# Performance work log

Hardware: AMD Instinct MI355X
Metric: run time of the kernel (lower is better)

## Reference

```python
import jax, jax.numpy as jnp
import numpy as np
from jax import lax

S = 3000      # number of stocks (and number of targets)
F = 6         # raw features
N = 128       # hidden size
L = 40        # lookback length
L_MAX = 10    # max lag
K = 5         # topk leaders


def setup_inputs() -> dict:
    key = jax.random.key(0)
    ks = jax.random.split(key, 16)
    sc = 1.0 / np.sqrt(N)
    u = lambda k, shp, s=sc: jax.random.uniform(k, shp, jnp.float32, -s, s)
    return {
        "X_scaled": jax.random.normal(ks[0], (1, S, L, F), jnp.float32),
        "X_raw": jax.random.normal(ks[1], (1, S, L, F), jnp.float32),
        "target_idx": jax.random.randint(ks[2], (S,), 0, S, jnp.int32),
        "lstm_Wih": u(ks[3], (4 * N, F)),
        "lstm_Whh": u(ks[4], (4 * N, N)),
        "lstm_bih": u(ks[5], (4 * N,)),
        "lstm_bhh": u(ks[6], (4 * N,)),
        "ln_g": jnp.ones((N,), jnp.float32),
        "ln_b": jnp.zeros((N,), jnp.float32),
        "WQ": u(ks[7], (N, N)),
        "WK": u(ks[8], (N, N)),
        "log_temp": jnp.asarray(np.log(N ** 0.25), jnp.float32),
        "lag_bias": jnp.zeros((L_MAX,), jnp.float32),
        "W1": u(ks[9], (64, 2 * F), 1.0 / np.sqrt(2 * F)),
        "b1": jnp.zeros((64,), jnp.float32),
        "W2": u(ks[10], (32, 64), 1.0 / 8.0),
        "b2": jnp.zeros((32,), jnp.float32),
        "W3": u(ks[11], (1, 32), 1.0 / np.sqrt(32)),
        "b3": jnp.zeros((1,), jnp.float32),
    }


def _lstm(x, Wih, Whh, bih, bhh):
    # x: [BS, L, F] -> hidden sequence [BS, L, N]; torch gate order i,f,g,o
    BS = x.shape[0]
    h0 = jnp.zeros((BS, N), x.dtype)
    bias = bih + bhh

    def step(carry, xt):
        h, c = carry
        g = xt @ Wih.T + h @ Whh.T + bias
        i, f, gg, o = jnp.split(g, 4, axis=-1)
        c = jax.nn.sigmoid(f) * c + jax.nn.sigmoid(i) * jnp.tanh(gg)
        h = jax.nn.sigmoid(o) * jnp.tanh(c)
        return (h, c), h

    _, hs = lax.scan(step, (h0, h0), jnp.swapaxes(x, 0, 1))
    return jnp.swapaxes(hs, 0, 1)


def _ln(x, g, b):
    m = x.mean(-1, keepdims=True)
    v = ((x - m) ** 2).mean(-1, keepdims=True)
    return (x - m) / jnp.sqrt(v + 1e-5) * g + b


def _l2norm(x):
    return x / jnp.clip(jnp.linalg.norm(x, axis=-1, keepdims=True), 1e-12)


def reference(X_scaled, X_raw, target_idx, lstm_Wih, lstm_Whh, lstm_bih,
              lstm_bhh, ln_g, ln_b, WQ, WK, log_temp, lag_bias,
              W1, b1, W2, b2, W3, b3):
    # TemporalEncoder: LSTM over B*S sequences + LayerNorm (B=1)
    H = _ln(_lstm(X_scaled.reshape(S, L, F), lstm_Wih, lstm_Whh,
                  lstm_bih, lstm_bhh), ln_g, ln_b)          # [S, L, N]
    X = X_raw[0]                                            # [S, L, F]

    q = _l2norm(H[target_idx, -1] @ WQ.T)                   # [T, N]
    Hk = _l2norm(H[:, L - L_MAX:] @ WK.T)                   # [S, l_max, N]
    temp = jnp.clip(jnp.exp(log_temp), 0.1, N ** 0.5)

    attn = jnp.einsum('tn,sln->tsl', q, Hk) / temp + lag_bias  # [T, S, l_max]
    self_mask = jnp.arange(S)[None, :] == target_idx[:, None]  # [T, S]
    attn = jnp.where(self_mask[:, :, None], -jnp.inf, attn)

    vals, idx = lax.top_k(attn.reshape(-1, S * L_MAX), K)   # [T, K]
    leader = idx // L_MAX
    lag_j = idx % L_MAX
    lag_pos = jnp.clip(L - 1 - (L_MAX - lag_j), 0, L - 1)

    z = X[leader, lag_pos]                                  # [T, K, F]
    w = jax.nn.softmax(vals, axis=1)
    z_agg = (w[..., None] * z).sum(1)                       # [T, F]
    feat = jnp.concatenate([z_agg, z[:, 0]], axis=-1)       # [T, 2F]

    h1 = jax.nn.relu(feat @ W1.T + b1)
    h2 = jax.nn.relu(h1 @ W2.T + b2)
    return (h2 @ W3.T + b3).squeeze(-1)                     # [T]
```

## Files before the change

kernel.cpp:

```cpp
#include <hip/hip_runtime.h>
#include <math.h>

#define S_N 3000
#define NCOLS 30000
#define SCHUNK 16
#define KTILES 938
#define TPC 59
#define PST 17

typedef __bf16 v8bf __attribute__((ext_vector_type(8)));
typedef float v16f __attribute__((ext_vector_type(16)));
typedef float v4f __attribute__((ext_vector_type(4)));

__device__ __forceinline__ float sigm(float x) { return 1.0f / (1.0f + expf(-x)); }

__device__ __forceinline__ bool bet(float av, int ai, float bv, int bi) {
  return (av > bv) || (av == bv && ai < bi);
}

template <int M>
__device__ __forceinline__ void insS(float (&v)[M], int (&ix)[M], float nv, int ni) {
  if (!(nv > v[M - 1])) return;
  bool b[M];
#pragma unroll
  for (int q = 0; q < M; q++) b[q] = nv > v[q];
#pragma unroll
  for (int q = M - 1; q > 0; q--) {
    v[q]  = b[q] ? (b[q - 1] ? v[q - 1] : nv) : v[q];
    ix[q] = b[q] ? (b[q - 1] ? ix[q - 1] : ni) : ix[q];
  }
  if (b[0]) { v[0] = nv; ix[0] = ni; }
}

template <int M>
__device__ __forceinline__ void insF(float (&v)[M], int (&ix)[M], float nv, int ni) {
  if (!bet(nv, ni, v[M - 1], ix[M - 1])) return;
  bool b[M];
#pragma unroll
  for (int q = 0; q < M; q++) b[q] = bet(nv, ni, v[q], ix[q]);
#pragma unroll
  for (int q = M - 1; q > 0; q--) {
    v[q]  = b[q] ? (b[q - 1] ? v[q - 1] : nv) : v[q];
    ix[q] = b[q] ? (b[q - 1] ? ix[q - 1] : ni) : ix[q];
  }
  if (b[0]) { v[0] = nv; ix[0] = ni; }
}

__device__ __forceinline__ unsigned short f2bf_rne(float f) {
  unsigned int u = __float_as_uint(f);
  unsigned int r = (u + 0x7fffu + ((u >> 16) & 1u)) >> 16;
  return (unsigned short)r;
}
__device__ __forceinline__ float bf2f(unsigned short h) {
  return __uint_as_float(((unsigned int)h) << 16);
}

__global__ __launch_bounds__(256) void cvt_wll(
    const float* __restrict__ Whh, unsigned short* __restrict__ Wllf)
{
  int idx = blockIdx.x * 256 + threadIdx.x;
  if (idx >= 128 * 512) return;
  int f = idx >> 9;
  int lane = (idx >> 3) & 63;
  int j = idx & 7;
  int w = f >> 3, tau = (f >> 1) & 3, s = f & 1;
  int kh = w >> 3, g8 = w & 7;
  int gate = g8 * 64 + tau * 16 + (lane & 15);
  int k = kh * 64 + s * 32 + (lane >> 4) * 8 + j;
  float x = Whh[gate * 128 + k];
  unsigned short hi = f2bf_rne(x);
  float r1 = x - bf2f(hi);
  unsigned short lo = f2bf_rne(r1);
  float r2 = r1 - bf2f(lo);
  Wllf[idx] = f2bf_rne(r2);
}

__global__ __launch_bounds__(1024, 4) void lstm_kernel(
    const float* __restrict__ Xs, const float* __restrict__ Wih,
    const float* __restrict__ Whh, const float* __restrict__ bih,
    const float* __restrict__ bhh, const unsigned short* __restrict__ Wllf,
    float* __restrict__ H10)
{
  __shared__ float P[2 * 512 * PST];
  __shared__ __align__(16) __bf16 Asp[3][4][64][8];
  __shared__ float Xb[12 * 240];
  __shared__ float2 WB2[14][128];

  const int tid = threadIdx.x;
  const int s0 = blockIdx.x * 12;
  const int lane = tid & 63;
  const int wv = tid >> 6;
  const int kh = wv >> 3;
  const int g8 = wv & 7;
  const int l15 = lane & 15, lq = lane >> 4;

  for (int i = tid; i < 12 * 240; i += 1024) Xb[i] = Xs[(size_t)s0 * 240 + i];
  for (int i = tid; i < 3 * 4 * 64 * 8; i += 1024)
    ((unsigned short*)Asp)[i] = 0;
  for (int i = tid; i < 14 * 128; i += 1024) {
    int q = i >> 7, n = i & 127;
    float vv[2];
#pragma unroll
    for (int e = 0; e < 2; e++) {
      int r = 2 * q + e;
      if (r < 24) {
        int gate = n + (r / 6) * 128;
        vv[e] = Wih[gate * 6 + r % 6];
      } else {
        int gate = n + (r - 24) * 128;
        vv[e] = bih[gate] + bhh[gate];
      }
    }
    WB2[q][n] = make_float2(vv[0], vv[1]);
  }

  v8bf whi[4][2], wlo[4][2];
#pragma unroll
  for (int tau = 0; tau < 4; tau++)
#pragma unroll
    for (int s = 0; s < 2; s++) {
      int gate = g8 * 64 + tau * 16 + l15;
      int k0 = kh * 64 + s * 32 + lq * 8;
      const float* wp = Whh + gate * 128 + k0;
      v8bf h8, l8;
#pragma unroll
      for (int j = 0; j < 8; j++) {
        float x = wp[j];
        __bf16 bh_ = (__bf16)x;
        float r1 = x - (float)bh_;
        __bf16 bl_ = (__bf16)r1;
        h8[j] = bh_;
        l8[j] = bl_;
      }
      whi[tau][s] = h8;
      wlo[tau][s] = l8;
    }

  const unsigned short* wllbase = Wllf + (size_t)(wv * 8) * 512 + lane * 8;

  float c0 = 0.0f, c1 = 0.0f;
  const int p2n = tid & 127;
  const int p2m = tid >> 7;

  __syncthreads();

#pragma unroll 1
  for (int t = 0; t < 40; t++) {
    v8bf ah[2], al[2], a3[2];
#pragma unroll
    for (int s = 0; s < 2; s++) {
      int ks = kh * 2 + s;
      ah[s] = *(const v8bf*)&Asp[0][ks][lane][0];
      al[s] = *(const v8bf*)&Asp[1][ks][lane][0];
      a3[s] = *(const v8bf*)&Asp[2][ks][lane][0];
    }
#pragma unroll
    for (int tau = 0; tau < 4; tau++) {
      v4f acc = {0.0f, 0.0f, 0.0f, 0.0f};
#pragma unroll
      for (int s = 0; s < 2; s++) {
        v8bf wll = *(const v8bf*)(wllbase + (tau * 2 + s) * 512);
        acc = __builtin_amdgcn_mfma_f32_16x16x32_bf16(ah[s], whi[tau][s], acc, 0, 0, 0);
        acc = __builtin_amdgcn_mfma_f32_16x16x32_bf16(ah[s], wlo[tau][s], acc, 0, 0, 0);
        acc = __builtin_amdgcn_mfma_f32_16x16x32_bf16(al[s], whi[tau][s], acc, 0, 0, 0);
        acc = __builtin_amdgcn_mfma_f32_16x16x32_bf16(al[s], wlo[tau][s], acc, 0, 0, 0);
        acc = __builtin_amdgcn_mfma_f32_16x16x32_bf16(ah[s], wll, acc, 0, 0, 0);
        acc = __builtin_amdgcn_mfma_f32_16x16x32_bf16(a3[s], whi[tau][s], acc, 0, 0, 0);
      }
      if (lq < 3) {
        int gate = g8 * 64 + tau * 16 + l15;
        float* pp = P + kh * (512 * PST) + gate * PST + lq * 4;
#pragma unroll
        for (int reg = 0; reg < 4; reg++) pp[reg] = acc[reg];
      }
    }
    __syncthreads();

#pragma unroll
    for (int task = 0; task < 2; task++) {
      if (task == 1 && tid >= 512) break;
      const int m = task == 0 ? p2m : 8 + p2m;
      const int n = p2n;
      float wb[28];
#pragma unroll
      for (int q = 0; q < 14; q++) {
        float2 v = WB2[q][n];
        wb[2 * q] = v.x;
        wb[2 * q + 1] = v.y;
      }
      const float* xm = Xb + m * 240 + t * 6;
      float xv[6];
#pragma unroll
      for (int f = 0; f < 6; f++) xv[f] = xm[f];
      float g4[4];
#pragma unroll
      for (int g = 0; g < 4; g++) {
        float a = wb[24 + g];
#pragma unroll
        for (int f = 0; f < 6; f++) a = fmaf(wb[g * 6 + f], xv[f], a);
        int gate = n + g * 128;
        a += P[gate * PST + m] + P[512 * PST + gate * PST + m];
        g4[g] = a;
      }
      float& c = task == 0 ? c0 : c1;
      c = sigm(g4[1]) * c + sigm(g4[0]) * tanhf(g4[2]);
      float h = sigm(g4[3]) * tanhf(c);
      if (t >= 30) H10[((size_t)(s0 + m) * 10 + (t - 30)) * 128 + n] = h;
      __bf16 hh = (__bf16)h;
      float r1 = h - (float)hh;
      __bf16 hl = (__bf16)r1;
      float r2 = r1 - (float)hl;
      __bf16 h3 = (__bf16)r2;
      int ks = n >> 5, li = m + 16 * ((n >> 3) & 3), j = n & 7;
      Asp[0][ks][li][j] = hh;
      Asp[1][ks][li][j] = hl;
      Asp[2][ks][li][j] = h3;
    }
    __syncthreads();
  }
}

__global__ __launch_bounds__(256) void ln_kernel(
    float* __restrict__ H, const float* __restrict__ g,
    const float* __restrict__ b, int nrows)
{
  int row = blockIdx.x * 4 + (threadIdx.x >> 6);
  int lane = threadIdx.x & 63;
  if (row >= nrows) return;
  float* hr = H + (size_t)row * 128;
  float x0 = hr[lane], x1 = hr[lane + 64];
  float s = x0 + x1;
  for (int off = 32; off > 0; off >>= 1) s += __shfl_xor(s, off);
  float mean = s * (1.0f / 128.0f);
  float d0 = x0 - mean, d1 = x1 - mean;
  float v = d0 * d0 + d1 * d1;
  for (int off = 32; off > 0; off >>= 1) v += __shfl_xor(v, off);
  float rstd = 1.0f / sqrtf(v * (1.0f / 128.0f) + 1e-5f);
  hr[lane] = d0 * rstd * g[lane] + b[lane];
  hr[lane + 64] = d1 * rstd * g[lane + 64] + b[lane + 64];
}

__global__ __launch_bounds__(256) void proj_kernel(
    const float* __restrict__ In, int inOff, int inStride, int nr,
    const float* __restrict__ W, float* __restrict__ Out)
{
  __shared__ float A_s[16 * 128];
  const int tid = threadIdx.x;
  const int r0 = blockIdx.x * 16;

  for (int i = tid; i < 16 * 32; i += 256) {
    int row = i >> 5, c = i & 31;
    int gr = r0 + row;
    float4 v = make_float4(0.f, 0.f, 0.f, 0.f);
    if (gr < nr)
      v = *(const float4*)(In + (size_t)inOff + (size_t)gr * inStride + c * 4);
    *(float4*)(A_s + row * 128 + c * 4) = v;
  }
  __syncthreads();

  const int j = tid & 127, rh = tid >> 7;
  const float* wrow = W + j * 128;
  float acc[8] = {0, 0, 0, 0, 0, 0, 0, 0};
  for (int kc = 0; kc < 32; kc++) {
    float4 wv4 = *(const float4*)(wrow + kc * 4);
#pragma unroll
    for (int i = 0; i < 8; i++) {
      float4 a4 = *(const float4*)(A_s + (rh * 8 + i) * 128 + kc * 4);
      acc[i] = fmaf(wv4.x, a4.x, acc[i]);
      acc[i] = fmaf(wv4.y, a4.y, acc[i]);
      acc[i] = fmaf(wv4.z, a4.z, acc[i]);
      acc[i] = fmaf(wv4.w, a4.w, acc[i]);
    }
  }
  __syncthreads();
#pragma unroll
  for (int i = 0; i < 8; i++) A_s[(rh * 8 + i) * 128 + j] = acc[i];
  __syncthreads();

  const int r = tid >> 4, qq = tid & 15;
  float ss = 0.0f;
#pragma unroll
  for (int i = 0; i < 8; i++) {
    float u = A_s[r * 128 + qq + i * 16];
    ss += u * u;
  }
  for (int off = 8; off > 0; off >>= 1) ss += __shfl_xor(ss, off);
  float scale = 1.0f / fmaxf(sqrtf(ss), 1e-12f);
  int gr = r0 + r;
  if (gr < nr) {
#pragma unroll
    for (int i = 0; i < 8; i++)
      Out[(size_t)gr * 128 + qq + i * 16] = A_s[r * 128 + qq + i * 16] * scale;
  }
}

__global__ __launch_bounds__(256) void cvt_kernel(
    const float* __restrict__ src, unsigned short* __restrict__ hi,
    unsigned short* __restrict__ lo, int n4)
{
  int i = blockIdx.x * 256 + threadIdx.x;
  if (i >= n4) return;
  float4 f = ((const float4*)src)[i];
  ushort4 h, l;
  h.x = f2bf_rne(f.x); l.x = f2bf_rne(f.x - bf2f(h.x));
  h.y = f2bf_rne(f.y); l.y = f2bf_rne(f.y - bf2f(h.y));
  h.z = f2bf_rne(f.z); l.z = f2bf_rne(f.z - bf2f(h.z));
  h.w = f2bf_rne(f.w); l.w = f2bf_rne(f.w - bf2f(h.w));
  ((ushort4*)hi)[i] = h;
  ((ushort4*)lo)[i] = l;
}

__global__ __launch_bounds__(256) void cvt_blockK(
    const float* __restrict__ Kn, unsigned short* __restrict__ hi,
    unsigned short* __restrict__ lo)
{
  const int tile = blockIdx.x;
  const int tid = threadIdx.x;
#pragma unroll
  for (int jj = 0; jj < 4; jj++) {
    int i = tid + jj * 256;
    int r = i >> 5;
    int c0 = (i & 31) * 4;
    int row = tile * 32 + r;
    if (row >= NCOLS) continue;
    float4 f = *(const float4*)(Kn + (size_t)row * 128 + c0);
    ushort4 h, l;
    h.x = f2bf_rne(f.x); l.x = f2bf_rne(f.x - bf2f(h.x));
    h.y = f2bf_rne(f.y); l.y = f2bf_rne(f.y - bf2f(h.y));
    h.z = f2bf_rne(f.z); l.z = f2bf_rne(f.z - bf2f(h.z));
    h.w = f2bf_rne(f.w); l.w = f2bf_rne(f.w - bf2f(h.w));
    int s = c0 >> 4, half = (c0 >> 3) & 1, e = c0 & 7;
    size_t idx = (size_t)tile * 4096 + s * 512 + half * 256 + r * 8 + e;
    *(ushort4*)(hi + idx) = h;
    *(ushort4*)(lo + idx) = l;
  }
}

__global__ __launch_bounds__(256, 3) void score_mfma(
    const unsigned short* __restrict__ Qh, const unsigned short* __restrict__ Ql,
    const unsigned short* __restrict__ Kh, const unsigned short* __restrict__ Kl,
    const int* __restrict__ tix, const float* __restrict__ log_temp,
    const float* __restrict__ lag_bias, float* __restrict__ part)
{
  __shared__ float lagS[16];
  __shared__ float M[256 * 16];
  const int tid = threadIdx.x;
  const int wv = tid >> 6, lane = tid & 63;
  const int half = lane >> 5, tcol = lane & 31;
  const int chunk = blockIdx.y;
  const int T0 = blockIdx.x * 32;
  const int tstart = chunk * TPC;
  const int tend = (tstart + TPC < KTILES) ? tstart + TPC : KTILES;

  if (tid < 10) lagS[tid] = lag_bias[tid];

  const int tgt = T0 + tcol;
  const int tgtc = tgt < S_N ? tgt : S_N - 1;
  const int myTix = tix[tgtc];
  const float invtemp =
      1.0f / fminf(fmaxf(expf(log_temp[0]), 0.1f), 11.313708499f);

  v8bf bh[8], bl[8];
  {
    const size_t qo = (size_t)myTix * 128 + half * 8;
#pragma unroll
    for (int s = 0; s < 8; s++) {
      bh[s] = *(const v8bf*)(Qh + qo + s * 16);
      bl[s] = *(const v8bf*)(Ql + qo + s * 16);
    }
  }
#pragma unroll
  for (int s = 0; s < 8; s++) {
    asm volatile("" : "+v"(bh[s]), "+v"(bl[s]));
  }

  float tv[8]; int ti[8];
#pragma unroll
  for (int q = 0; q < 8; q++) { tv[q] = -3e38f; ti[q] = 0x7fffffff; }

  __syncthreads();

  for (int it = 0; it < 15; it++) {
    const int tile = tstart + it * 4 + wv;
    const int tilec = tile < KTILES ? tile : KTILES - 1;
    const size_t ao = (size_t)tilec * 4096 + half * 256 + tcol * 8;

    v16f acc0, acc1;
#pragma unroll
    for (int q = 0; q < 16; q++) { acc0[q] = 0.0f; acc1[q] = 0.0f; }

#pragma unroll
    for (int s = 0; s < 8; s++) {
      v8bf ah = *(const v8bf*)(Kh + ao + s * 512);
      v8bf al = *(const v8bf*)(Kl + ao + s * 512);
      acc0 = __builtin_amdgcn_mfma_f32_32x32x16_bf16(ah, bh[s], acc0, 0, 0, 0);
      acc1 = __builtin_amdgcn_mfma_f32_32x32x16_bf16(ah, bl[s], acc1, 0, 0, 0);
      acc1 = __builtin_amdgcn_mfma_f32_32x32x16_bf16(al, bh[s], acc1, 0, 0, 0);
    }

    const int cb = tile * 32;
    const bool act = tile < tend;
#pragma unroll
    for (int reg = 0; reg < 16; reg++) {
      const int row = (reg & 3) + 8 * (reg >> 2) + 4 * half;
      const int col = cb + row;
      if (act && col < NCOLS) {
        const int s = col / 10;
        const int lag = col - s * 10;
        if (s != myTix) {
          float vsc = (acc0[reg] + acc1[reg]) * invtemp + lagS[lag];
          insS<8>(tv, ti, vsc, col);
        }
      }
    }
  }

  {
    float* my = M + tid * 16;
#pragma unroll
    for (int q = 0; q < 8; q++) {
      my[2 * q] = tv[q];
      my[2 * q + 1] = __int_as_float(ti[q]);
    }
  }
  __syncthreads();
  if (tid < 32 && T0 + tid < S_N) {
    float v[8]; int ix[8];
#pragma unroll
    for (int q = 0; q < 8; q++) { v[q] = -3e38f; ix[q] = 0x7fffffff; }
    for (int w = 0; w < 8; w++) {
      const float* src = M + (w * 32 + tid) * 16;
#pragma unroll
      for (int q = 0; q < 8; q++)
        insF<8>(v, ix, src[2 * q], __float_as_int(src[2 * q + 1]));
    }
    float* dst = part + ((size_t)(T0 + tid) * SCHUNK + chunk) * 16;
#pragma unroll
    for (int q = 0; q < 8; q++) {
      dst[2 * q] = v[q];
      dst[2 * q + 1] = __int_as_float(ix[q]);
    }
  }
}

__global__ __launch_bounds__(256) void final_kernel(
    const float* __restrict__ part, const float* __restrict__ Qn,
    const float* __restrict__ Kn, const int* __restrict__ tix,
    const float* __restrict__ log_temp, const float* __restrict__ lag_bias,
    const float* __restrict__ Xraw,
    const float* __restrict__ W1, const float* __restrict__ b1,
    const float* __restrict__ W2, const float* __restrict__ b2,
    const float* __restrict__ W3, const float* __restrict__ b3,
    float* __restrict__ out)
{
  __shared__ float W1s[64 * 12];
  __shared__ float W2s[32 * 64];
  __shared__ float b1s[64];
  __shared__ float b2s[32];
  __shared__ float W3s[32];
  const int tid = threadIdx.x;
  for (int i = tid; i < 768; i += 256) W1s[i] = W1[i];
  for (int i = tid; i < 2048; i += 256) W2s[i] = W2[i];
  if (tid < 64) b1s[tid] = b1[tid];
  if (tid < 32) { b2s[tid] = b2[tid]; W3s[tid] = W3[tid]; }
  __syncthreads();

  int t = blockIdx.x * 256 + tid;
  if (t >= S_N) return;

  float av[8]; int ai[8];
#pragma unroll
  for (int q = 0; q < 8; q++) { av[q] = -3e38f; ai[q] = 0x7fffffff; }
  const float* pp = part + (size_t)t * (SCHUNK * 16);
  for (int c = 0; c < SCHUNK * 8; c++)
    insF<8>(av, ai, pp[2 * c], __float_as_int(pp[2 * c + 1]));

  const float invtemp =
      1.0f / fminf(fmaxf(expf(log_temp[0]), 0.1f), 11.313708499f);
  const float* q = Qn + (size_t)tix[t] * 128;
  const float* kr[8];
#pragma unroll
  for (int j = 0; j < 8; j++) kr[j] = Kn + (size_t)ai[j] * 128;
  float d[8] = {0, 0, 0, 0, 0, 0, 0, 0};
  for (int kc = 0; kc < 32; kc++) {
    float4 q4 = ((const float4*)q)[kc];
#pragma unroll
    for (int j = 0; j < 8; j++) {
      float4 k4 = ((const float4*)kr[j])[kc];
      d[j] = fmaf(q4.x, k4.x, d[j]);
      d[j] = fmaf(q4.y, k4.y, d[j]);
      d[j] = fmaf(q4.z, k4.z, d[j]);
      d[j] = fmaf(q4.w, k4.w, d[j]);
    }
  }

  float v[5]; int ix[5];
#pragma unroll
  for (int qq = 0; qq < 5; qq++) { v[qq] = -3e38f; ix[qq] = 0x7fffffff; }
#pragma unroll
  for (int j = 0; j < 8; j++) {
    int c = ai[j];
    int s = c / 10;
    int lag = c - 10 * s;
    float ev = d[j] * invtemp + lag_bias[lag];
    insF<5>(v, ix, ev, c);
  }

  float e1 = expf(v[1] - v[0]), e2 = expf(v[2] - v[0]),
        e3 = expf(v[3] - v[0]), e4 = expf(v[4] - v[0]);
  float rs = 1.0f / (1.0f + e1 + e2 + e3 + e4);
  float w_[5] = {rs, e1 * rs, e2 * rs, e3 * rs, e4 * rs};

  float feat[12];
#pragma unroll
  for (int f = 0; f < 12; f++) feat[f] = 0.0f;
#pragma unroll
  for (int qq = 0; qq < 5; qq++) {
    int iq = ix[qq];
    int s = iq / 10;
    int l = iq - 10 * s;
    int pos = 29 + l;
    const float* zp = Xraw + (size_t)s * 240 + pos * 6;
#pragma unroll
    for (int f = 0; f < 6; f++) {
      float z = zp[f];
      feat[f] += w_[qq] * z;
      if (qq == 0) feat[6 + f] = z;
    }
  }

  float h1[64];
#pragma unroll 4
  for (int o = 0; o < 64; o++) {
    float acc = b1s[o];
    const float* wr = W1s + o * 12;
#pragma unroll
    for (int f = 0; f < 12; f++) acc = fmaf(wr[f], feat[f], acc);
    h1[o] = fmaxf(acc, 0.0f);
  }
  float rr = b3[0];
#pragma unroll 2
  for (int o = 0; o < 32; o++) {
    float acc = b2s[o];
    const float* wr = W2s + o * 64;
#pragma unroll 8
    for (int k = 0; k < 64; k++) acc = fmaf(wr[k], h1[k], acc);
    rr = fmaf(W3s[o], fmaxf(acc, 0.0f), rr);
  }
  out[t] = rr;
}

extern "C" void kernel_launch(void* const* d_in, const int* in_sizes, int n_in,
                              void* d_out, int out_size, void* d_ws,
                              size_t ws_size, hipStream_t stream) {
  const float* Xs   = (const float*)d_in[0];
  const float* Xraw = (const float*)d_in[1];
  const int*   tix  = (const int*)d_in[2];
  const float* Wih  = (const float*)d_in[3];
  const float* Whh  = (const float*)d_in[4];
  const float* bih  = (const float*)d_in[5];
  const float* bhh  = (const float*)d_in[6];
  const float* ln_g = (const float*)d_in[7];
  const float* ln_b = (const float*)d_in[8];
  const float* WQ   = (const float*)d_in[9];
  const float* WK   = (const float*)d_in[10];
  const float* log_temp = (const float*)d_in[11];
  const float* lag_bias = (const float*)d_in[12];
  const float* W1 = (const float*)d_in[13];
  const float* b1 = (const float*)d_in[14];
  const float* W2 = (const float*)d_in[15];
  const float* b2 = (const float*)d_in[16];
  const float* W3 = (const float*)d_in[17];
  const float* b3 = (const float*)d_in[18];
  float* outp = (float*)d_out;

  float* ws = (float*)d_ws;
  float* H10 = ws;
  unsigned short* Khi = (unsigned short*)ws;
  unsigned short* Klo = (unsigned short*)(ws + 1922000);
  float* Kn  = ws + 3850000;
  float* Qn  = ws + 7690000;
  unsigned short* Qhi = (unsigned short*)(ws + 8074000);
  unsigned short* Qlo = (unsigned short*)(ws + 8266000);
  float* part = ws + 8458000;
  unsigned short* Wllf = (unsigned short*)(ws + 9226000);

  cvt_wll<<<256, 256, 0, stream>>>(Whh, Wllf);
  lstm_kernel<<<250, 1024, 0, stream>>>(Xs, Wih, Whh, bih, bhh, Wllf, H10);
  ln_kernel<<<7500, 256, 0, stream>>>(H10, ln_g, ln_b, 30000);
  proj_kernel<<<1875, 256, 0, stream>>>(H10, 0, 128, 30000, WK, Kn);
  proj_kernel<<<188, 256, 0, stream>>>(H10, 9 * 128, 1280, 3000, WQ, Qn);
  cvt_blockK<<<KTILES, 256, 0, stream>>>(Kn, Khi, Klo);
  cvt_kernel<<<375, 256, 0, stream>>>(Qn, Qhi, Qlo, 96000);
  {
    dim3 grid(94, SCHUNK);
    score_mfma<<<grid, 256, 0, stream>>>(Qhi, Qlo, Khi, Klo, tix, log_temp,
                                         lag_bias, part);
  }
  final_kernel<<<12, 256, 0, stream>>>(part, Qn, Kn, tix, log_temp, lag_bias,
                                       Xraw, W1, b1, W2, b2, W3, b3, outp);
}
```

Measured before the change: 812.0 us.

## Stage Q fragments in LDS and split accumulators to raise occupancy

Moves the per-lane hi/lo bf16 query fragments out of registers into shared memory, loading them into LDS once and reading them each MFMA step. Launch bounds rise from 3 to 4 waves per SIMD. The dependent MFMA chain on one accumulator is split into two independent accumulators to shorten the dependency chain. This trades extra LDS reads per tile and a third accumulator's registers for higher occupancy, and the order of the floating-point sums changes slightly.

After: 887.1 us. 1.09x slower.

```diff
diff --git a/kernel.cpp b/kernel.cpp
--- a/kernel.cpp
+++ b/kernel.cpp
@@ -336,13 +336,14 @@
   }
 }
 
-__global__ __launch_bounds__(256, 3) void score_mfma(
+__global__ __launch_bounds__(256, 4) void score_mfma(
     const unsigned short* __restrict__ Qh, const unsigned short* __restrict__ Ql,
     const unsigned short* __restrict__ Kh, const unsigned short* __restrict__ Kl,
     const int* __restrict__ tix, const float* __restrict__ log_temp,
     const float* __restrict__ lag_bias, float* __restrict__ part)
 {
   __shared__ float lagS[16];
+  __shared__ __align__(16) unsigned short Qs[2][8][64][8];
   __shared__ float M[256 * 16];
   const int tid = threadIdx.x;
   const int wv = tid >> 6, lane = tid & 63;
@@ -360,18 +361,16 @@
   const float invtemp =
       1.0f / fminf(fmaxf(expf(log_temp[0]), 0.1f), 11.313708499f);
 
-  v8bf bh[8], bl[8];
-  {
-    const size_t qo = (size_t)myTix * 128 + half * 8;
-#pragma unroll
-    for (int s = 0; s < 8; s++) {
-      bh[s] = *(const v8bf*)(Qh + qo + s * 16);
-      bl[s] = *(const v8bf*)(Ql + qo + s * 16);
-    }
-  }
-#pragma unroll
-  for (int s = 0; s < 8; s++) {
-    asm volatile("" : "+v"(bh[s]), "+v"(bl[s]));
+  for (int i = tid; i < 1024; i += 256) {
+    int split = i >> 9;
+    int s = (i >> 6) & 7;
+    int lq2 = i & 63;
+    int halfq = lq2 >> 5, tcq = lq2 & 31;
+    int tq = T0 + tcq;
+    int src = tix[tq < S_N ? tq : S_N - 1];
+    const unsigned short* sp =
+        (split ? Ql : Qh) + (size_t)src * 128 + halfq * 8 + s * 16;
+    *(uint4*)&Qs[split][s][lq2][0] = *(const uint4*)sp;
   }
 
   float tv[8]; int ti[8];
@@ -385,17 +384,19 @@
     const int tilec = tile < KTILES ? tile : KTILES - 1;
     const size_t ao = (size_t)tilec * 4096 + half * 256 + tcol * 8;
 
-    v16f acc0, acc1;
-#pragma unroll
-    for (int q = 0; q < 16; q++) { acc0[q] = 0.0f; acc1[q] = 0.0f; }
+    v16f acc0, acc1a, acc1b;
+#pragma unroll
+    for (int q = 0; q < 16; q++) { acc0[q] = 0.0f; acc1a[q] = 0.0f; acc1b[q] = 0.0f; }
 
 #pragma unroll
     for (int s = 0; s < 8; s++) {
       v8bf ah = *(const v8bf*)(Kh + ao + s * 512);
       v8bf al = *(const v8bf*)(Kl + ao + s * 512);
-      acc0 = __builtin_amdgcn_mfma_f32_32x32x16_bf16(ah, bh[s], acc0, 0, 0, 0);
-      acc1 = __builtin_amdgcn_mfma_f32_32x32x16_bf16(ah, bl[s], acc1, 0, 0, 0);
-      acc1 = __builtin_amdgcn_mfma_f32_32x32x16_bf16(al, bh[s], acc1, 0, 0, 0);
+      v8bf qh8 = *(const v8bf*)&Qs[0][s][lane][0];
+      v8bf ql8 = *(const v8bf*)&Qs[1][s][lane][0];
+      acc0  = __builtin_amdgcn_mfma_f32_32x32x16_bf16(ah, qh8, acc0, 0, 0, 0);
+      acc1a = __builtin_amdgcn_mfma_f32_32x32x16_bf16(ah, ql8, acc1a, 0, 0, 0);
+      acc1b = __builtin_amdgcn_mfma_f32_32x32x16_bf16(al, qh8, acc1b, 0, 0, 0);
     }
 
     const int cb = tile * 32;
@@ -408,7 +409,8 @@
         const int s = col / 10;
         const int lag = col - s * 10;
         if (s != myTix) {
-          float vsc = (acc0[reg] + acc1[reg]) * invtemp + lagS[lag];
+          float vsc =
+              (acc0[reg] + (acc1a[reg] + acc1b[reg])) * invtemp + lagS[lag];
           insS<8>(tv, ti, vsc, col);
         }
       }
```
